# Performance work log

Hardware: AMD Instinct MI355X
Metric: run time of the kernel (lower is better)

## Reference

```python
import jax, jax.numpy as jnp
import numpy as np

L, D, H, FF, I, MAXREL = 6, 512, 8, 2048, 50, 128
HD = D // H
NREL = 2 * MAXREL + 1
EPS = 1e-5


def setup_inputs() -> dict:
    key = jax.random.key(0)
    ks = jax.random.split(key, 32)
    s = 0.02
    p = {
        'x': jax.random.normal(ks[0], (16, 512, I), dtype=jnp.float32),
        'in_w': jax.random.normal(ks[1], (I, D)) * s,
        'in_b': jnp.zeros((D,), jnp.float32),
        'Wq': jax.random.normal(ks[2], (L, D, D)) * s,
        'Wk': jax.random.normal(ks[3], (L, D, D)) * s,
        'Wv': jax.random.normal(ks[4], (L, D, D)) * s,
        'Wo': jax.random.normal(ks[5], (L, D, D)) * s,
        'bo': jnp.zeros((L, D), jnp.float32),
        'rel_emb': jax.random.normal(ks[6], (L, NREL, HD)) * s,
        'w1': jax.random.normal(ks[7], (L, D, FF)) * s,
        'b1': jnp.zeros((L, FF), jnp.float32),
        'w2': jax.random.normal(ks[8], (L, FF, D)) * s,
        'b2': jnp.zeros((L, D), jnp.float32),
        'ln1_g': jnp.ones((L, D), jnp.float32),
        'ln1_b': jnp.zeros((L, D), jnp.float32),
        'ln2_g': jnp.ones((L, D), jnp.float32),
        'ln2_b': jnp.zeros((L, D), jnp.float32),
        'on_g': jnp.ones((D,), jnp.float32),
        'on_b': jnp.zeros((D,), jnp.float32),
        'p1_w': jax.random.normal(ks[9], (D, D // 2)) * s,
        'p1_b': jnp.zeros((D // 2,), jnp.float32),
        'p2_w': jax.random.normal(ks[10], (D // 2, 1)) * s,
        'p2_b': jnp.zeros((1,), jnp.float32),
    }
    return p


def _layer_norm(x, g, b):
    m = jnp.mean(x, axis=-1, keepdims=True)
    v = jnp.mean(jnp.square(x - m), axis=-1, keepdims=True)
    return (x - m) * jax.lax.rsqrt(v + EPS) * g + b


def _sinusoidal_pe(seq_len, d_model):
    pos = jnp.arange(seq_len, dtype=jnp.float32)[:, None]
    div = jnp.exp(jnp.arange(0, d_model, 2, dtype=jnp.float32) * (-jnp.log(10000.0) / d_model))
    pe = jnp.zeros((seq_len, d_model), jnp.float32)
    pe = pe.at[:, 0::2].set(jnp.sin(pos * div))
    pe = pe.at[:, 1::2].set(jnp.cos(pos * div))
    return pe


def reference(x, in_w, in_b, Wq, Wk, Wv, Wo, bo, rel_emb, w1, b1, w2, b2,
              ln1_g, ln1_b, ln2_g, ln2_b, on_g, on_b, p1_w, p1_b, p2_w, p2_b):
    B, S, _ = x.shape
    scale = jnp.sqrt(jnp.float32(HD))
    # relative position index matrix [S, S] in [0, 2*MAXREL]
    r = jnp.arange(S)
    rel_idx = jnp.clip(r[None, :] - r[:, None], -MAXREL, MAXREL) + MAXREL

    h = x @ in_w + in_b                       # [B,S,D]
    h = h + _sinusoidal_pe(S, D)

    for l in range(L):
        q = (h @ Wq[l]).reshape(B, S, H, HD).transpose(0, 2, 1, 3)  # [B,H,S,hd]
        k = (h @ Wk[l]).reshape(B, S, H, HD).transpose(0, 2, 1, 3)
        v = (h @ Wv[l]).reshape(B, S, H, HD).transpose(0, 2, 1, 3)
        scores = jnp.einsum('bhqd,bhkd->bhqk', q, k) / scale
        rel = rel_emb[l][rel_idx]             # [S,S,hd]
        scores = scores + jnp.einsum('bhqd,qkd->bhqk', q, rel)  # rel bias is NOT scaled (matches source)
        attn = jax.nn.softmax(scores, axis=-1)
        ctx = jnp.einsum('bhqk,bhkd->bhqd', attn, v)
        ctx = ctx.transpose(0, 2, 1, 3).reshape(B, S, D)
        attn_out = ctx @ Wo[l] + bo[l]
        h = _layer_norm(h + attn_out, ln1_g[l], ln1_b[l])
        ff = jax.nn.relu(h @ w1[l] + b1[l]) @ w2[l] + b2[l]
        h = _layer_norm(h + ff, ln2_g[l], ln2_b[l])

    h = _layer_norm(h, on_g, on_b)
    out = jax.nn.relu(h @ p1_w + p1_b) @ p2_w + p2_b  # [B,S,1]
    return out
```

## Files before the change

### kernel.cpp

```cpp
#include <hip/hip_runtime.h>

typedef unsigned short u16;
typedef unsigned int   u32;
typedef short   short8  __attribute__((ext_vector_type(8)));
typedef float   floatx4 __attribute__((ext_vector_type(4)));
typedef int     intx4   __attribute__((ext_vector_type(4)));

#define NTOK 8192
#define SEQ  512
#define NLAYER 6

#define OFF_WT   ((size_t)0)
#define OFF_HB   ((size_t)38010880)
#define OFF_QKV  ((size_t)46399488)
#define OFF_CTX  ((size_t)71565312)
#define OFF_GOUT ((size_t)79953920)
#define OFF_FF   ((size_t)96731136)
#define OFF_HD1  ((size_t)130285568)
#define OFF_VT   OFF_FF
#define OFF_RELB OFF_HD1

#define LSTRIDE 3145728
#define P1T_OFF 18874368

__device__ __forceinline__ float b2f(u16 v) { return __uint_as_float(((u32)v) << 16); }
__device__ __forceinline__ float lo16(u32 v) { return __uint_as_float(v << 16); }
__device__ __forceinline__ float hi16(u32 v) { return __uint_as_float(v & 0xffff0000u); }
__device__ __forceinline__ u16 f2b(float f) {
  u32 x = __float_as_uint(f);
  return (u16)((x + 0x7fffu + ((x >> 16) & 1u)) >> 16);
}
__device__ __forceinline__ u32 pack2(float a, float b) {
  return (u32)f2b(a) | ((u32)f2b(b) << 16);
}
__device__ __forceinline__ u32 cvtpk(float a, float b) {
  u32 r;
  asm("v_cvt_pk_bf16_f32 %0, %1, %2" : "=v"(r) : "v"(a), "v"(b));
  return r;
}

typedef __attribute__((address_space(1))) void* gas_t;
typedef __attribute__((address_space(3))) void* las_t;

__global__ __launch_bounds__(256) void transpose_all(
    const float* __restrict__ Wq, const float* __restrict__ Wk,
    const float* __restrict__ Wv, const float* __restrict__ Wo,
    const float* __restrict__ w1, const float* __restrict__ w2,
    const float* __restrict__ p1, u16* __restrict__ wT)
{
  __shared__ u16 tile[64][65];
  const int tb = blockIdx.x;
  const float* src; u16* dst; int R, C, tidx;
  if (tb < 4608) {
    const int l = tb / 768, r = tb % 768;
    const size_t lofs = (size_t)l * LSTRIDE;
    if (r < 256) {
      const int m = r >> 6; tidx = r & 63; R = 512; C = 512;
      const float* bases[4] = {Wq, Wk, Wv, Wo};
      src = bases[m] + (size_t)l * 262144;
      dst = wT + lofs + (size_t)m * 262144;
    } else if (r < 512) {
      tidx = r - 256; R = 512; C = 2048;
      src = w1 + (size_t)l * 1048576; dst = wT + lofs + 1048576;
    } else {
      tidx = r - 512; R = 2048; C = 512;
      src = w2 + (size_t)l * 1048576; dst = wT + lofs + 2097152;
    }
  } else {
    tidx = tb - 4608; R = 512; C = 256;
    src = p1; dst = wT + P1T_OFF;
  }
  const int tcn = C >> 6;
  const int tr = tidx / tcn, tc = tidx % tcn;
  const int th = threadIdx.x;
  {
    const int lr = th >> 2, cg = (th & 3) * 16;
    const float* sp = src + (size_t)(tr*64 + lr) * C + tc*64 + cg;
    float4 f0 = *(const float4*)(sp);
    float4 f1 = *(const float4*)(sp + 4);
    float4 f2 = *(const float4*)(sp + 8);
    float4 f3 = *(const float4*)(sp + 12);
    u16* tp = &tile[lr][cg];
    tp[0]=f2b(f0.x); tp[1]=f2b(f0.y); tp[2]=f2b(f0.z); tp[3]=f2b(f0.w);
    tp[4]=f2b(f1.x); tp[5]=f2b(f1.y); tp[6]=f2b(f1.z); tp[7]=f2b(f1.w);
    tp[8]=f2b(f2.x); tp[9]=f2b(f2.y); tp[10]=f2b(f2.z); tp[11]=f2b(f2.w);
    tp[12]=f2b(f3.x); tp[13]=f2b(f3.y); tp[14]=f2b(f3.z); tp[15]=f2b(f3.w);
  }
  __syncthreads();
  {
    const int oc = th >> 2, rg = (th & 3) * 16;
    u32 wds[8];
    #pragma unroll
    for (int i = 0; i < 8; ++i)
      wds[i] = (u32)tile[rg + 2*i][oc] | ((u32)tile[rg + 2*i + 1][oc] << 16);
    u16* dp = dst + (size_t)(tc*64 + oc) * R + tr*64 + rg;
    uint4 o0; o0.x=wds[0]; o0.y=wds[1]; o0.z=wds[2]; o0.w=wds[3];
    uint4 o1; o1.x=wds[4]; o1.y=wds[5]; o1.z=wds[6]; o1.w=wds[7];
    *(uint4*)dp = o0;
    *(uint4*)(dp + 8) = o1;
  }
}

__global__ __launch_bounds__(128) void input_proj(
    const float* __restrict__ x, const float* __restrict__ w, const float* __restrict__ ib,
    u16* __restrict__ hb)
{
  const int row = blockIdx.x, t = threadIdx.x;
  const int s = row & (SEQ - 1);
  __shared__ float xs[50];
  if (t < 50) xs[t] = x[row*50 + t];
  __syncthreads();
  const int d0 = t * 4;
  float4 acc = *(const float4*)(ib + d0);
  #pragma unroll
  for (int i = 0; i < 50; ++i) {
    const float4 wv = *(const float4*)(w + i*512 + d0);
    const float xv = xs[i];
    acc.x = fmaf(xv, wv.x, acc.x);
    acc.y = fmaf(xv, wv.y, acc.y);
    acc.z = fmaf(xv, wv.z, acc.z);
    acc.w = fmaf(xv, wv.w, acc.w);
  }
  const float cexp = -0.017988946f;
  const float dv0 = __expf((float)d0 * cexp);
  const float dv1 = __expf((float)(d0 + 2) * cexp);
  float s0, c0, s1, c1;
  __sincosf((float)s * dv0, &s0, &c0);
  __sincosf((float)s * dv1, &s1, &c1);
  acc.x += s0; acc.y += c0; acc.z += s1; acc.w += c1;
  u32* hp = (u32*)(hb + (size_t)row*512 + d0);
  hp[0] = pack2(acc.x, acc.y);
  hp[1] = pack2(acc.z, acc.w);
}

__global__ __launch_bounds__(256, 2) void gemm_bt(
    const u16* __restrict__ A, const u16* __restrict__ Bt,
    const float* __restrict__ bias,
    float* __restrict__ outF0, float* __restrict__ outF1, u16* __restrict__ outB,
    u16* __restrict__ vTout,
    const int M, const int N, const int K, const int kLen, const int flags)
{
  __shared__ __align__(16) u16 As[2][8192];
  __shared__ __align__(16) u16 Bs[2][8192];
  const int id = blockIdx.x;
  const int xcd = id & 7, rest = id >> 3;
  const int bm = (rest & 7) * 8 + xcd;
  const int bn = rest >> 3;
  const int z = blockIdx.y;
  const int kOff = z * kLen;
  const int m0 = bm << 7, n0 = bn << 7;
  const int tid = threadIdx.x;
  const int wave = tid >> 6, lane = tid & 63;
  const int wr = (wave >> 1) << 6, wc = (wave & 1) << 6;
  const int lrow = lane & 15, lquad = lane >> 4;

  floatx4 acc[4][4];
  #pragma unroll
  for (int i = 0; i < 4; ++i)
    #pragma unroll
    for (int j = 0; j < 4; ++j) { floatx4 zz = {0.f,0.f,0.f,0.f}; acc[i][j] = zz; }

  const u16* a0p = A  + (size_t)m0 * K + kOff;
  const u16* b0p = Bt + (size_t)n0 * K + kOff;
  const int c0 = tid, c1 = 256 + tid;
  const int ar0 = c0 >> 2, as0 = (c0 & 3) * 8;
  const int ar1 = c1 >> 2, as1 = (c1 & 3) * 8;

#define STAGE_G(buf, k0) do {                                                                  \
    __builtin_amdgcn_global_load_lds((gas_t)(a0p + (size_t)ar0*K + (k0) + as0),                \
                                     (las_t)(&As[buf][c0*8]), 16, 0, 0);                       \
    __builtin_amdgcn_global_load_lds((gas_t)(a0p + (size_t)ar1*K + (k0) + as1),                \
                                     (las_t)(&As[buf][c1*8]), 16, 0, 0);                       \
    __builtin_amdgcn_global_load_lds((gas_t)(b0p + (size_t)ar0*K + (k0) + as0),                \
                                     (las_t)(&Bs[buf][c0*8]), 16, 0, 0);                       \
    __builtin_amdgcn_global_load_lds((gas_t)(b0p + (size_t)ar1*K + (k0) + as1),                \
                                     (las_t)(&Bs[buf][c1*8]), 16, 0, 0);                       \
    __builtin_amdgcn_global_load_lds((gas_t)(a0p + (size_t)ar0*K + (k0) + 32 + as0),           \
                                     (las_t)(&As[buf][4096 + c0*8]), 16, 0, 0);                \
    __builtin_amdgcn_global_load_lds((gas_t)(a0p + (size_t)ar1*K + (k0) + 32 + as1),           \
                                     (las_t)(&As[buf][4096 + c1*8]), 16, 0, 0);                \
    __builtin_amdgcn_global_load_lds((gas_t)(b0p + (size_t)ar0*K + (k0) + 32 + as0),           \
                                     (las_t)(&Bs[buf][4096 + c0*8]), 16, 0, 0);                \
    __builtin_amdgcn_global_load_lds((gas_t)(b0p + (size_t)ar1*K + (k0) + 32 + as1),           \
                                     (las_t)(&Bs[buf][4096 + c1*8]), 16, 0, 0);                \
  } while (0)

  const int nst = kLen >> 6;
  STAGE_G(0, 0);
  __syncthreads();

  int cur = 0;
  for (int t = 0; t < nst; ++t) {
    if (t + 1 < nst) STAGE_G(cur ^ 1, (t + 1) * 64);
    #pragma unroll
    for (int hh = 0; hh < 2; ++hh) {
      short8 af[4], bf[4];
      #pragma unroll
      for (int i = 0; i < 4; ++i) af[i] = *(const short8*)&As[cur][hh*4096 + (wr + i*16 + lrow)*32 + lquad*8];
      #pragma unroll
      for (int j = 0; j < 4; ++j) bf[j] = *(const short8*)&Bs[cur][hh*4096 + (wc + j*16 + lrow)*32 + lquad*8];
      #pragma unroll
      for (int i = 0; i < 4; ++i)
        #pragma unroll
        for (int j = 0; j < 4; ++j)
          acc[i][j] = __builtin_amdgcn_mfma_f32_16x16x32_bf16(bf[j], af[i], acc[i][j], 0, 0, 0);
    }
    if (t + 1 < nst) { __syncthreads(); cur ^= 1; }
  }
#undef STAGE_G

  if ((flags & 4) && n0 >= 1024) {
    #pragma unroll
    for (int i = 0; i < 4; ++i) {
      const int row = m0 + wr + i*16 + lrow;
      const int bb = row >> 9, s = row & 511;
      #pragma unroll
      for (int j = 0; j < 4; ++j) {
        const int cm0 = (n0 - 1024) + wc + j*16 + lquad*4;
        #pragma unroll
        for (int v = 0; v < 4; ++v) {
          const int cm = cm0 + v;
          const int hh = cm >> 6, d = cm & 63;
          vTout[((size_t)(bb*8 + hh)*64 + d)*512 + s] = f2b(acc[i][j][v]);
        }
      }
    }
    return;
  }

  float* outF = (z == 0) ? outF0 : outF1;
  const bool hasb = ((flags & 1) != 0) && (z == 0);
  const bool dorelu = (flags & 2) != 0;
  #pragma unroll
  for (int i = 0; i < 4; ++i) {
    const int row = m0 + wr + i*16 + lrow;
    #pragma unroll
    for (int j = 0; j < 4; ++j) {
      const int colbase = n0 + wc + j*16 + lquad*4;
      float4 bv4 = make_float4(0.f, 0.f, 0.f, 0.f);
      if (hasb) bv4 = *(const float4*)(bias + colbase);
      float v0 = acc[i][j][0] + bv4.x;
      float v1 = acc[i][j][1] + bv4.y;
      float v2 = acc[i][j][2] + bv4.z;
      float v3 = acc[i][j][3] + bv4.w;
      if (dorelu) {
        v0 = fmaxf(v0, 0.f); v1 = fmaxf(v1, 0.f);
        v2 = fmaxf(v2, 0.f); v3 = fmaxf(v3, 0.f);
      }
      const size_t off = (size_t)row * N + colbase;
      if (outB) {
        uint2 o; o.x = pack2(v0, v1); o.y = pack2(v2, v3);
        *(uint2*)(outB + off) = o;
      } else {
        *(float4*)(outF + off) = make_float4(v0, v1, v2, v3);
      }
    }
  }
}

__global__ __launch_bounds__(256) void cvt_rel_all(
    const float* __restrict__ rel, u16* __restrict__ relB)
{
  const int i = blockIdx.x*256 + threadIdx.x;
  if (i < 6*257*64) {
    const int l = i / 16448, rem = i % 16448;
    relB[l*17408 + rem] = f2b(rel[i]);
  }
}

__global__ __launch_bounds__(256, 3) void attn_mfma(
    const u16* __restrict__ qkv, const u16* __restrict__ vT,
    const u16* __restrict__ relB, u16* __restrict__ ctx)
{
  const int id = blockIdx.x;
  const int xcd = id & 7, g = (id >> 3) & 15, qt = id >> 7;
  const int bh = xcd*16 + g;
  const int b = bh >> 3, h = bh & 7;
  const int t = threadIdx.x, w = t >> 6, lane = t & 63;
  const int lr = lane & 15, quad = lane >> 4;

  __shared__ __align__(16) u16 Ks[64*72];
  __shared__ __align__(16) u16 Vs[64*72];
  __shared__ __align__(16) u16 Pr[64*274];

  const size_t token0 = (size_t)b*512 + qt*64;
  const int srow = t >> 2, scol = (t & 3) * 16;
  const u16* kbase = qkv + (size_t)b*512*1536 + 512 + h*64;
  const u16* vbase = vT + (size_t)bh*64*512;

  short8 af0, af1;
  {
    const u16* qp = qkv + (token0 + w*16 + lr)*1536 + h*64 + quad*8;
    af0 = *(const short8*)(qp);
    af1 = *(const short8*)(qp + 32);
  }

  uint4 kr0, kr1, vr0, vr1;
  {
    const u16* kp = kbase + (size_t)srow*1536 + scol;
    kr0 = *(const uint4*)kp; kr1 = *(const uint4*)(kp + 8);
    const u16* vp = vbase + (size_t)srow*512 + scol;
    vr0 = *(const uint4*)vp; vr1 = *(const uint4*)(vp + 8);
  }

  #pragma unroll 4
  for (int nt = 0; nt < 17; ++nt) {
    const u16* rp = relB + (nt*16 + lr)*64 + quad*8;
    short8 rb0 = *(const short8*)(rp);
    short8 rb1 = *(const short8*)(rp + 32);
    floatx4 c = {0.f,0.f,0.f,0.f};
    c = __builtin_amdgcn_mfma_f32_16x16x32_bf16(af0, rb0, c, 0, 0, 0);
    c = __builtin_amdgcn_mfma_f32_16x16x32_bf16(af1, rb1, c, 0, 0, 0);
    #pragma unroll
    for (int r = 0; r < 4; ++r)
      Pr[(w*16 + quad*4 + r)*274 + nt*16 + lr] = f2b(c[r] * 1.44269504f);
  }

  floatx4 oacc[4];
  float lacc = 0.f;
  #pragma unroll
  for (int n = 0; n < 4; ++n) { floatx4 zz = {0.f,0.f,0.f,0.f}; oacc[n] = zz; }

  const int qglob = qt*64 + w*16 + lr;
  const int prbase = (w*16 + lr)*274 + 128;

  for (int kt = 0; kt < 8; ++kt) {
    __syncthreads();
    *(uint4*)&Ks[srow*72 + scol]     = kr0;
    *(uint4*)&Ks[srow*72 + scol + 8] = kr1;
    *(uint4*)&Vs[srow*72 + scol]     = vr0;
    *(uint4*)&Vs[srow*72 + scol + 8] = vr1;
    __syncthreads();

    if (kt < 7) {
      const u16* kp = kbase + (size_t)((kt+1)*64 + srow)*1536 + scol;
      kr0 = *(const uint4*)kp; kr1 = *(const uint4*)(kp + 8);
      const u16* vp = vbase + (size_t)srow*512 + (kt+1)*64 + scol;
      vr0 = *(const uint4*)vp; vr1 = *(const uint4*)(vp + 8);
    }

    floatx4 s4[4];
    __builtin_amdgcn_s_setprio(1);
    #pragma unroll
    for (int nt = 0; nt < 4; ++nt) {
      short8 kb0 = *(const short8*)&Ks[(nt*16 + lr)*72 + quad*8];
      short8 kb1 = *(const short8*)&Ks[(nt*16 + lr)*72 + 32 + quad*8];
      floatx4 c = {0.f,0.f,0.f,0.f};
      c = __builtin_amdgcn_mfma_f32_16x16x32_bf16(kb0, af0, c, 0, 0, 0);
      c = __builtin_amdgcn_mfma_f32_16x16x32_bf16(kb1, af1, c, 0, 0, 0);
      s4[nt] = c;
    }
    __builtin_amdgcn_s_setprio(0);

    u32 wq[4][2];
    const int kq = kt*64 + quad*4 - qglob;
    #pragma unroll
    for (int nt = 0; nt < 4; ++nt) {
      const int dbase = kq + nt*16;
      float p[4];
      #pragma unroll
      for (int r = 0; r < 4; ++r) {
        int dd = dbase + r;
        dd = dd < -128 ? -128 : (dd > 128 ? 128 : dd);
        p[r] = exp2f(fmaf(s4[nt][r], 0.18033688f, b2f(Pr[prbase + dd])));
      }
      lacc += (p[0] + p[1]) + (p[2] + p[3]);
      wq[nt][0] = cvtpk(p[0], p[1]);
      wq[nt][1] = cvtpk(p[2], p[3]);
    }

    intx4 pw0; pw0.x = (int)wq[0][0]; pw0.y = (int)wq[0][1];
               pw0.z = (int)wq[1][0]; pw0.w = (int)wq[1][1];
    intx4 pw1; pw1.x = (int)wq[2][0]; pw1.y = (int)wq[2][1];
               pw1.z = (int)wq[3][0]; pw1.w = (int)wq[3][1];
    const short8 pf0 = __builtin_bit_cast(short8, pw0);
    const short8 pf1 = __builtin_bit_cast(short8, pw1);

    __builtin_amdgcn_s_setprio(1);
    #pragma unroll
    for (int nd = 0; nd < 4; ++nd) {
      const int vrow = (nd*16 + lr)*72;
      uint2 a0 = *(const uint2*)&Vs[vrow + quad*4];
      uint2 a1 = *(const uint2*)&Vs[vrow + 16 + quad*4];
      uint2 a2 = *(const uint2*)&Vs[vrow + 32 + quad*4];
      uint2 a3 = *(const uint2*)&Vs[vrow + 48 + quad*4];
      intx4 v0; v0.x = (int)a0.x; v0.y = (int)a0.y; v0.z = (int)a1.x; v0.w = (int)a1.y;
      intx4 v1; v1.x = (int)a2.x; v1.y = (int)a2.y; v1.z = (int)a3.x; v1.w = (int)a3.y;
      const short8 vb0 = __builtin_bit_cast(short8, v0);
      const short8 vb1 = __builtin_bit_cast(short8, v1);
      oacc[nd] = __builtin_amdgcn_mfma_f32_16x16x32_bf16(vb0, pf0, oacc[nd], 0, 0, 0);
      oacc[nd] = __builtin_amdgcn_mfma_f32_16x16x32_bf16(vb1, pf1, oacc[nd], 0, 0, 0);
    }
    __builtin_amdgcn_s_setprio(0);
  }

  lacc += __shfl_xor(lacc, 16);
  lacc += __shfl_xor(lacc, 32);

  {
    const float inv = 1.f / lacc;
    u16* cp = ctx + (token0 + w*16 + lr)*512 + h*64;
    #pragma unroll
    for (int nd = 0; nd < 4; ++nd) {
      const int d = nd*16 + quad*4;
      uint2 o;
      o.x = pack2(oacc[nd][0]*inv, oacc[nd][1]*inv);
      o.y = pack2(oacc[nd][2]*inv, oacc[nd][3]*inv);
      *(uint2*)(cp + d) = o;
    }
  }
}

__global__ __launch_bounds__(128) void ln_kernel(
    const u16* __restrict__ resB, const float* __restrict__ add0,
    const float* __restrict__ add1,
    const float* __restrict__ g, const float* __restrict__ be,
    u16* __restrict__ hb)
{
  const int row = blockIdx.x, t = threadIdx.x;
  const size_t base = (size_t)row * 512;
  const u32 r0 = *(const u32*)(resB + base + t*4);
  const u32 r1 = *(const u32*)(resB + base + t*4 + 2);
  float x0 = lo16(r0), x1 = hi16(r0), x2 = lo16(r1), x3 = hi16(r1);
  if (add0) {
    const float4 a = *(const float4*)(add0 + base + t*4);
    x0 += a.x; x1 += a.y; x2 += a.z; x3 += a.w;
  }
  if (add1) {
    const float4 a = *(const float4*)(add1 + base + t*4);
    x0 += a.x; x1 += a.y; x2 += a.z; x3 += a.w;
  }
  float s = x0 + x1 + x2 + x3;
  #pragma unroll
  for (int off = 32; off > 0; off >>= 1) s += __shfl_down(s, off);
  __shared__ float red[2];
  const int wv = t >> 6, ln = t & 63;
  if (ln == 0) red[wv] = s;
  __syncthreads();
  const float mean = (red[0] + red[1]) * (1.f/512.f);
  const float dx0 = x0-mean, dx1 = x1-mean, dx2 = x2-mean, dx3 = x3-mean;
  float vs = dx0*dx0 + dx1*dx1 + dx2*dx2 + dx3*dx3;
  __syncthreads();
  #pragma unroll
  for (int off = 32; off > 0; off >>= 1) vs += __shfl_down(vs, off);
  if (ln == 0) red[wv] = vs;
  __syncthreads();
  const float var = (red[0] + red[1]) * (1.f/512.f);
  const float inv = 1.f / sqrtf(var + 1e-5f);
  const float4 gv = *(const float4*)(g + t*4);
  const float4 bv = *(const float4*)(be + t*4);
  const float y0 = dx0*inv*gv.x + bv.x;
  const float y1 = dx1*inv*gv.y + bv.y;
  const float y2 = dx2*inv*gv.z + bv.z;
  const float y3 = dx3*inv*gv.w + bv.w;
  u32* hp = (u32*)(hb + base + t*4);
  hp[0] = pack2(y0, y1); hp[1] = pack2(y2, y3);
}

__global__ __launch_bounds__(256) void head2_kernel(
    const u16* __restrict__ hd1, const float* __restrict__ p2w,
    const float* __restrict__ p2b, float* __restrict__ out)
{
  const int wv = threadIdx.x >> 6, ln = threadIdx.x & 63;
  const int row = blockIdx.x * 4 + wv;
  const u16* hp = hd1 + (size_t)row * 256 + ln*4;
  const u32 h0 = *(const u32*)hp, h1 = *(const u32*)(hp + 2);
  const float4 w = *(const float4*)(p2w + ln*4);
  float acc = lo16(h0)*w.x + hi16(h0)*w.y + lo16(h1)*w.z + hi16(h1)*w.w;
  #pragma unroll
  for (int off = 1; off < 64; off <<= 1) acc += __shfl_xor(acc, off);
  if (ln == 0) out[row] = acc + p2b[0];
}

extern "C" void kernel_launch(void* const* d_in, const int* in_sizes, int n_in,
                              void* d_out, int out_size, void* d_ws, size_t ws_size,
                              hipStream_t stream) {
  (void)in_sizes; (void)n_in; (void)out_size; (void)ws_size;
  const float* X    = (const float*)d_in[0];
  const float* INW  = (const float*)d_in[1];
  const float* INB  = (const float*)d_in[2];
  const float* WQ   = (const float*)d_in[3];
  const float* WK   = (const float*)d_in[4];
  const float* WV   = (const float*)d_in[5];
  const float* WO   = (const float*)d_in[6];
  const float* BO   = (const float*)d_in[7];
  const float* REL  = (const float*)d_in[8];
  const float* W1   = (const float*)d_in[9];
  const float* B1   = (const float*)d_in[10];
  const float* W2   = (const float*)d_in[11];
  const float* B2   = (const float*)d_in[12];
  const float* LN1G = (const float*)d_in[13];
  const float* LN1B = (const float*)d_in[14];
  const float* LN2G = (const float*)d_in[15];
  const float* LN2B = (const float*)d_in[16];
  const float* ONG  = (const float*)d_in[17];
  const float* ONB  = (const float*)d_in[18];
  const float* P1W  = (const float*)d_in[19];
  const float* P1B  = (const float*)d_in[20];
  const float* P2W  = (const float*)d_in[21];
  const float* P2B  = (const float*)d_in[22];
  float* out = (float*)d_out;

  char* ws = (char*)d_ws;
  u16*   wT    = (u16*)(ws + OFF_WT);
  u16*   hB    = (u16*)(ws + OFF_HB);
  u16*   qkv   = (u16*)(ws + OFF_QKV);
  u16*   ctx   = (u16*)(ws + OFF_CTX);
  float* gout0 = (float*)(ws + OFF_GOUT);
  float* gout1 = (float*)(ws + OFF_QKV);
  u16*   ff    = (u16*)(ws + OFF_FF);
  u16*   hd1   = (u16*)(ws + OFF_HD1);
  u16*   vTb   = (u16*)(ws + OFF_VT);
  u16*   relBa = (u16*)(ws + OFF_RELB);

  transpose_all<<<4640, 256, 0, stream>>>(WQ, WK, WV, WO, W1, W2, P1W, wT);
  cvt_rel_all<<<386, 256, 0, stream>>>(REL, relBa);
  input_proj<<<NTOK, 128, 0, stream>>>(X, INW, INB, hB);

  for (int l = 0; l < NLAYER; ++l) {
    const u16* wTl = wT + (size_t)l * LSTRIDE;
    gemm_bt<<<dim3(768,1), 256, 0, stream>>>(hB, wTl, nullptr, nullptr, nullptr, qkv, vTb,
                                             8192, 1536, 512, 512, 4);
    attn_mfma<<<1024, 256, 0, stream>>>(qkv, vTb, relBa + l*17408, ctx);
    gemm_bt<<<dim3(256,2), 256, 0, stream>>>(ctx, wTl + 786432, BO + l*512,
                                             gout0, gout1, nullptr, nullptr,
                                             8192, 512, 512, 256, 1);
    ln_kernel<<<NTOK, 128, 0, stream>>>(hB, gout0, gout1, LN1G + l*512, LN1B + l*512, hB);
    gemm_bt<<<dim3(1024,1), 256, 0, stream>>>(hB, wTl + 1048576, B1 + l*2048,
                                              nullptr, nullptr, ff, nullptr,
                                              8192, 2048, 512, 512, 3);
    gemm_bt<<<dim3(256,2), 256, 0, stream>>>(ff, wTl + 2097152, B2 + l*512,
                                             gout0, gout1, nullptr, nullptr,
                                             8192, 512, 2048, 1024, 1);
    ln_kernel<<<NTOK, 128, 0, stream>>>(hB, gout0, gout1, LN2G + l*512, LN2B + l*512, hB);
  }
  ln_kernel<<<NTOK, 128, 0, stream>>>(hB, nullptr, nullptr, ONG, ONB, hB);
  gemm_bt<<<dim3(128,1), 256, 0, stream>>>(hB, wT + P1T_OFF, P1B,
                                           nullptr, nullptr, hd1, nullptr,
                                           8192, 256, 512, 512, 3);
  head2_kernel<<<2048, 256, 0, stream>>>(hd1, P2W, P2B, out);
}
```

Baseline: 1.142 ms.

## Pre-swizzle weights into MFMA fragment layout and load B directly to registers

The weight transpose kernel now writes the bf16 weights in a blocked layout that matches the MFMA B-fragment order per 128-column tile and 32-wide k chunk. The GEMM drops its B shared-memory buffer and each wave loads its B fragments straight from global memory with coalesced 16-byte loads. This halves LDS use and raises the occupancy hint to 4 blocks per CU. The cost is that B reuse across the two waves sharing columns now goes through cache instead of LDS, and global load latency sits directly in the MFMA loop.

```diff
diff --git a/kernel.cpp b/kernel.cpp
--- a/kernel.cpp
+++ b/kernel.cpp
@@ -93,11 +93,16 @@
     #pragma unroll
     for (int i = 0; i < 8; ++i)
       wds[i] = (u32)tile[rg + 2*i][oc] | ((u32)tile[rg + 2*i + 1][oc] << 16);
-    u16* dp = dst + (size_t)(tc*64 + oc) * R + tr*64 + rg;
+    const int n  = tc*64 + oc;
+    const int k0 = tr*64 + rg;
+    const int nb = n >> 7, j = (n >> 4) & 7, lr = n & 15;
+    const int kc = k0 >> 5, lq = (k0 >> 3) & 3;
+    const int KC = R >> 5;
+    u16* base = dst + (((((size_t)nb*KC + kc) << 3) + j) << 9);
     uint4 o0; o0.x=wds[0]; o0.y=wds[1]; o0.z=wds[2]; o0.w=wds[3];
     uint4 o1; o1.x=wds[4]; o1.y=wds[5]; o1.z=wds[6]; o1.w=wds[7];
-    *(uint4*)dp = o0;
-    *(uint4*)(dp + 8) = o1;
+    *(uint4*)(base + (lq*16 + lr)*8)       = o0;
+    *(uint4*)(base + ((lq+1)*16 + lr)*8)   = o1;
   }
 }
 
@@ -133,7 +138,7 @@
   hp[1] = pack2(acc.z, acc.w);
 }
 
-__global__ __launch_bounds__(256, 2) void gemm_bt(
+__global__ __launch_bounds__(256, 4) void gemm_bt(
     const u16* __restrict__ A, const u16* __restrict__ Bt,
     const float* __restrict__ bias,
     float* __restrict__ outF0, float* __restrict__ outF1, u16* __restrict__ outB,
@@ -141,7 +146,6 @@
     const int M, const int N, const int K, const int kLen, const int flags)
 {
   __shared__ __align__(16) u16 As[2][8192];
-  __shared__ __align__(16) u16 Bs[2][8192];
   const int id = blockIdx.x;
   const int xcd = id & 7, rest = id >> 3;
   const int bm = (rest & 7) * 8 + xcd;
@@ -160,54 +164,60 @@
     #pragma unroll
     for (int j = 0; j < 4; ++j) { floatx4 zz = {0.f,0.f,0.f,0.f}; acc[i][j] = zz; }
 
-  const u16* a0p = A  + (size_t)m0 * K + kOff;
-  const u16* b0p = Bt + (size_t)n0 * K + kOff;
+  const u16* a0p = A + (size_t)m0 * K + kOff;
   const int c0 = tid, c1 = 256 + tid;
   const int ar0 = c0 >> 2, as0 = (c0 & 3) * 8;
   const int ar1 = c1 >> 2, as1 = (c1 & 3) * 8;
-
-#define STAGE_G(buf, k0) do {                                                                  \
+  const int KC = K >> 5;
+  const u16* bW = Bt + ((((size_t)bn*KC + (kOff >> 5)) * 8 + (wave & 1) * 4) << 9) + lane*8;
+
+#define STAGE_A(buf, k0) do {                                                                  \
     __builtin_amdgcn_global_load_lds((gas_t)(a0p + (size_t)ar0*K + (k0) + as0),                \
                                      (las_t)(&As[buf][c0*8]), 16, 0, 0);                       \
     __builtin_amdgcn_global_load_lds((gas_t)(a0p + (size_t)ar1*K + (k0) + as1),                \
                                      (las_t)(&As[buf][c1*8]), 16, 0, 0);                       \
-    __builtin_amdgcn_global_load_lds((gas_t)(b0p + (size_t)ar0*K + (k0) + as0),                \
-                                     (las_t)(&Bs[buf][c0*8]), 16, 0, 0);                       \
-    __builtin_amdgcn_global_load_lds((gas_t)(b0p + (size_t)ar1*K + (k0) + as1),                \
-                                     (las_t)(&Bs[buf][c1*8]), 16, 0, 0);                       \
     __builtin_amdgcn_global_load_lds((gas_t)(a0p + (size_t)ar0*K + (k0) + 32 + as0),           \
                                      (las_t)(&As[buf][4096 + c0*8]), 16, 0, 0);                \
     __builtin_amdgcn_global_load_lds((gas_t)(a0p + (size_t)ar1*K + (k0) + 32 + as1),           \
                                      (las_t)(&As[buf][4096 + c1*8]), 16, 0, 0);                \
-    __builtin_amdgcn_global_load_lds((gas_t)(b0p + (size_t)ar0*K + (k0) + 32 + as0),           \
-                                     (las_t)(&Bs[buf][4096 + c0*8]), 16, 0, 0);                \
-    __builtin_amdgcn_global_load_lds((gas_t)(b0p + (size_t)ar1*K + (k0) + 32 + as1),           \
-                                     (las_t)(&Bs[buf][4096 + c1*8]), 16, 0, 0);                \
   } while (0)
 
   const int nst = kLen >> 6;
-  STAGE_G(0, 0);
+  STAGE_A(0, 0);
   __syncthreads();
 
   int cur = 0;
   for (int t = 0; t < nst; ++t) {
-    if (t + 1 < nst) STAGE_G(cur ^ 1, (t + 1) * 64);
-    #pragma unroll
-    for (int hh = 0; hh < 2; ++hh) {
-      short8 af[4], bf[4];
+    const u16* bc = bW + (size_t)(2*t) * 4096;
+    short8 b0[4], b1[4];
+    #pragma unroll
+    for (int j = 0; j < 4; ++j) b0[j] = *(const short8*)(bc + j*512);
+    if (t + 1 < nst) STAGE_A(cur ^ 1, (t + 1) * 64);
+    #pragma unroll
+    for (int j = 0; j < 4; ++j) b1[j] = *(const short8*)(bc + 4096 + j*512);
+    {
+      short8 af[4];
       #pragma unroll
-      for (int i = 0; i < 4; ++i) af[i] = *(const short8*)&As[cur][hh*4096 + (wr + i*16 + lrow)*32 + lquad*8];
-      #pragma unroll
-      for (int j = 0; j < 4; ++j) bf[j] = *(const short8*)&Bs[cur][hh*4096 + (wc + j*16 + lrow)*32 + lquad*8];
+      for (int i = 0; i < 4; ++i) af[i] = *(const short8*)&As[cur][(wr + i*16 + lrow)*32 + lquad*8];
       #pragma unroll
       for (int i = 0; i < 4; ++i)
         #pragma unroll
         for (int j = 0; j < 4; ++j)
-          acc[i][j] = __builtin_amdgcn_mfma_f32_16x16x32_bf16(bf[j], af[i], acc[i][j], 0, 0, 0);
+          acc[i][j] = __builtin_amdgcn_mfma_f32_16x16x32_bf16(b0[j], af[i], acc[i][j], 0, 0, 0);
+    }
+    {
+      short8 af[4];
+      #pragma unroll
+      for (int i = 0; i < 4; ++i) af[i] = *(const short8*)&As[cur][4096 + (wr + i*16 + lrow)*32 + lquad*8];
+      #pragma unroll
+      for (int i = 0; i < 4; ++i)
+        #pragma unroll
+        for (int j = 0; j < 4; ++j)
+          acc[i][j] = __builtin_amdgcn_mfma_f32_16x16x32_bf16(b1[j], af[i], acc[i][j], 0, 0, 0);
     }
     if (t + 1 < nst) { __syncthreads(); cur ^= 1; }
   }
-#undef STAGE_G
+#undef STAGE_A
 
   if ((flags & 4) && n0 >= 1024) {
     #pragma unroll
```

Result: faster. 1.104 ms (-3.3%).
